# Optimization experiments

Hardware: AMD Instinct MI355X
Metric: run time of the kernel (lower is better)

Reference implementation:

```python
import jax, jax.numpy as jnp
import numpy as np

D_MODEL, D_STATE, D_EVENT, BATCH = 2048, 16, 32, 2048


def setup_inputs() -> dict:
    key = jax.random.key(0)
    ks = jax.random.split(key, 16)
    s = lambda k, sh, scale=0.02: jax.random.normal(k, sh, dtype=jnp.float32) * scale
    # A_log init as in torch: log(idx/d_state*0.5 + 0.05), expanded over d_model
    idx = jnp.arange(1, D_STATE + 1, dtype=jnp.float32)
    A_log = jnp.broadcast_to(jnp.log(idx / D_STATE * 0.5 + 0.05)[None, :], (D_MODEL, D_STATE)).copy()
    return {
        "x_t": jax.random.normal(ks[0], (BATCH, D_MODEL), dtype=jnp.float32),
        "h_prev": jax.random.normal(ks[1], (BATCH, D_MODEL, D_STATE), dtype=jnp.float32),
        "event_t": jax.random.normal(ks[2], (BATCH, D_EVENT), dtype=jnp.float32),
        "A_log": A_log,
        "D": jnp.ones((D_MODEL,), dtype=jnp.float32),
        "Wd": s(ks[3], (D_MODEL, D_MODEL)),
        "bd": jax.random.uniform(ks[4], (D_MODEL,), minval=-2.0, maxval=-1.0, dtype=jnp.float32),
        "We": s(ks[5], (D_MODEL, D_EVENT)),
        "B_W1": s(ks[6], (2 * D_STATE, D_MODEL)),
        "B_b1": jnp.zeros((2 * D_STATE,), dtype=jnp.float32),
        "B_W2": s(ks[7], (D_STATE, 2 * D_STATE)),
        "B_b2": jnp.zeros((D_STATE,), dtype=jnp.float32),
        "B_We": s(ks[8], (D_STATE, D_EVENT)),
        "A_We": s(ks[9], (D_MODEL, D_EVENT)),
        "C_W": s(ks[10], (D_STATE, D_MODEL)),
    }


def reference(x_t, h_prev, event_t, A_log, D, Wd, bd, We, B_W1, B_b1, B_W2, B_b2, B_We, A_We, C_W):
    # event-modulated step size: (B, d_model)
    delta = jax.nn.softplus(x_t @ Wd.T + bd + event_t @ We.T)
    # input-to-state matrix: (B, d_state)
    B_t = jax.nn.silu(x_t @ B_W1.T + B_b1) @ B_W2.T + B_b2 + event_t @ B_We.T
    C_t = x_t @ C_W.T  # (B, d_state)
    A_base = -jnp.exp(jnp.clip(A_log, -3.0, 1.0))[None]        # (1, d_model, d_state)
    event_pole = (event_t @ A_We.T)[..., None]                  # (B, d_model, 1)
    A_eff = A_base + event_pole                                 # (B, d_model, d_state)
    delta_safe = jnp.minimum(delta, 2.0)[..., None]             # (B, d_model, 1)
    A_bar = jnp.exp(delta_safe * A_eff)
    B_bar = delta_safe * B_t[:, None, :]                        # (B, d_model, d_state)
    h_t = A_bar * h_prev + B_bar * x_t[..., None]
    y_t = jnp.einsum('bdn,bn->bd', h_t, C_t) + D * x_t
    return (y_t, h_t)
```

## Files before the change

### kernel.cpp

```cpp
#include <hip/hip_runtime.h>
#include <math.h>

#define D_MODEL 2048
#define D_STATE 16
#define D_EVENT 32
#define BATCH   2048

typedef __attribute__((ext_vector_type(4))) float f32x4;
typedef __attribute__((ext_vector_type(8))) short short8;
typedef __attribute__((ext_vector_type(8))) __bf16 bf16x8;
typedef __attribute__((ext_vector_type(4))) unsigned short us4;

__device__ inline unsigned short f2bf(float f) {
  unsigned int u = __builtin_bit_cast(unsigned int, f);
  u += 0x7fffu + ((u >> 16) & 1u);
  return (unsigned short)(u >> 16);
}

__global__ __launch_bounds__(256) void prep_kernel(
    const float* __restrict__ x, const float* __restrict__ wd,
    const float* __restrict__ ev, const float* __restrict__ we,
    const float* __restrict__ alog,
    unsigned short* __restrict__ xb, unsigned short* __restrict__ wdb,
    unsigned short* __restrict__ evb, unsigned short* __restrict__ web,
    float* __restrict__ abase)
{
  const int t = blockIdx.x * 256 + threadIdx.x;
  if (t < (BATCH * D_MODEL) / 4) {
    f32x4 v = *(const f32x4*)(x + (size_t)t * 4);
    f32x4 w = *(const f32x4*)(wd + (size_t)t * 4);
    us4 ov, ow;
#pragma unroll
    for (int r = 0; r < 4; ++r) { ov[r] = f2bf(v[r]); ow[r] = f2bf(w[r]); }
    *(us4*)(xb + (size_t)t * 4) = ov;
    *(us4*)(wdb + (size_t)t * 4) = ow;
  }
  if (t < (BATCH * D_EVENT) / 4) {
    f32x4 e = *(const f32x4*)(ev + (size_t)t * 4);
    f32x4 s = *(const f32x4*)(we + (size_t)t * 4);
    us4 oe, os;
#pragma unroll
    for (int r = 0; r < 4; ++r) { oe[r] = f2bf(e[r]); os[r] = f2bf(s[r]); }
    *(us4*)(evb + (size_t)t * 4) = oe;
    *(us4*)(web + (size_t)t * 4) = os;
  }
  if (t < (D_MODEL * D_STATE) / 4) {
    f32x4 a = *(const f32x4*)(alog + (size_t)t * 4);
    f32x4 o;
#pragma unroll
    for (int r = 0; r < 4; ++r) {
      float c = fminf(fmaxf(a[r], -3.0f), 1.0f);
      o[r] = -expf(c);
    }
    *(f32x4*)(abase + (size_t)t * 4) = o;
  }
}

__global__ __launch_bounds__(256) void bc_kernel(
    const float* __restrict__ x, const float* __restrict__ ev,
    const float* __restrict__ BW1, const float* __restrict__ Bb1,
    const float* __restrict__ BW2, const float* __restrict__ Bb2,
    const float* __restrict__ BWe, const float* __restrict__ CW,
    float* __restrict__ Bt, float* __restrict__ Ct)
{
  __shared__ float xs[D_MODEL];
  __shared__ float t1s[2 * D_STATE];
  const int b = blockIdx.x, tid = threadIdx.x;
  f32x4* xs4 = (f32x4*)xs;
  const f32x4* xg = (const f32x4*)(x + (size_t)b * D_MODEL);
  xs4[tid] = xg[tid];
  xs4[tid + 256] = xg[tid + 256];
  __syncthreads();
  const int wave = tid >> 6, lane = tid & 63;
#pragma unroll 1
  for (int jj = 0; jj < 12; ++jj) {
    const int j = wave * 12 + jj;
    const float* wr = (j < 32) ? (BW1 + (size_t)j * D_MODEL)
                               : (CW + (size_t)(j - 32) * D_MODEL);
    float s = 0.f;
    for (int k = lane; k < D_MODEL; k += 64) s += xs[k] * wr[k];
#pragma unroll
    for (int o = 32; o > 0; o >>= 1) s += __shfl_xor(s, o);
    if (lane == 0) {
      if (j < 32) {
        float z = s + Bb1[j];
        t1s[j] = z / (1.f + expf(-z));
      } else {
        Ct[b * D_STATE + (j - 32)] = s;
      }
    }
  }
  __syncthreads();
  if (tid < D_STATE) {
    const int n = tid;
    float s = Bb2[n];
    const float* w2 = BW2 + n * (2 * D_STATE);
    const float* we = BWe + n * D_EVENT;
    const float* eb = ev + (size_t)b * D_EVENT;
#pragma unroll
    for (int k = 0; k < 2 * D_STATE; ++k) s += t1s[k] * w2[k];
#pragma unroll
    for (int k = 0; k < D_EVENT; ++k) s += eb[k] * we[k];
    Bt[b * D_STATE + n] = s;
  }
}

__device__ inline void gld_lds16(const unsigned short* g, unsigned short* l) {
  __builtin_amdgcn_global_load_lds(
      (const __attribute__((address_space(1))) unsigned int*)g,
      (__attribute__((address_space(3))) unsigned int*)l, 16, 0, 0);
}

__global__ __launch_bounds__(256) void gemm_delta(
    const unsigned short* __restrict__ xb, const unsigned short* __restrict__ wdb,
    const unsigned short* __restrict__ evb, const unsigned short* __restrict__ web,
    const float* __restrict__ bd, float* __restrict__ delta)
{
  __shared__ unsigned short As[128 * 32];
  __shared__ unsigned short Bs[128 * 32];
  const int tid = threadIdx.x;
  const int wave = tid >> 6, lane = tid & 63;
  const int r16 = lane & 15, q = lane >> 4;
  const int b0 = blockIdx.y * 128, d0 = blockIdx.x * 128;
  const int wm = (wave >> 1) * 64, wn = (wave & 1) * 64;
  const int srow = tid >> 2, skp = tid & 3;
  f32x4 acc[4][4] = {};

  for (int kt = 0; kt < D_MODEL / 32; ++kt) {
    const int k0 = kt * 32;
#pragma unroll
    for (int c = 0; c < 2; ++c) {
      gld_lds16(xb + (size_t)(b0 + srow + c * 64) * D_MODEL + k0 + skp * 8,
                As + c * 2048 + wave * 512);
      gld_lds16(wdb + (size_t)(d0 + srow + c * 64) * D_MODEL + k0 + skp * 8,
                Bs + c * 2048 + wave * 512);
    }
    __syncthreads();
    bf16x8 af[4], bf[4];
#pragma unroll
    for (int i = 0; i < 4; ++i) {
      af[i] = __builtin_bit_cast(bf16x8, *(const short8*)(As + (wm + i * 16 + r16) * 32 + q * 8));
      bf[i] = __builtin_bit_cast(bf16x8, *(const short8*)(Bs + (wn + i * 16 + r16) * 32 + q * 8));
    }
#pragma unroll
    for (int i = 0; i < 4; ++i)
#pragma unroll
      for (int j = 0; j < 4; ++j)
        acc[i][j] = __builtin_amdgcn_mfma_f32_16x16x32_bf16(af[i], bf[j], acc[i][j], 0, 0, 0);
    __syncthreads();
  }
  {
#pragma unroll
    for (int c = 0; c < 2; ++c) {
      gld_lds16(evb + (size_t)(b0 + srow + c * 64) * D_EVENT + skp * 8,
                As + c * 2048 + wave * 512);
      gld_lds16(web + (size_t)(d0 + srow + c * 64) * D_EVENT + skp * 8,
                Bs + c * 2048 + wave * 512);
    }
    __syncthreads();
    bf16x8 af[4], bf[4];
#pragma unroll
    for (int i = 0; i < 4; ++i) {
      af[i] = __builtin_bit_cast(bf16x8, *(const short8*)(As + (wm + i * 16 + r16) * 32 + q * 8));
      bf[i] = __builtin_bit_cast(bf16x8, *(const short8*)(Bs + (wn + i * 16 + r16) * 32 + q * 8));
    }
#pragma unroll
    for (int i = 0; i < 4; ++i)
#pragma unroll
      for (int j = 0; j < 4; ++j)
        acc[i][j] = __builtin_amdgcn_mfma_f32_16x16x32_bf16(af[i], bf[j], acc[i][j], 0, 0, 0);
  }
#pragma unroll
  for (int j = 0; j < 4; ++j) {
    const int d = d0 + wn + j * 16 + r16;
    const float bdv = bd[d];
#pragma unroll
    for (int i = 0; i < 4; ++i) {
      const int brow = b0 + wm + i * 16 + q * 4;
#pragma unroll
      for (int r = 0; r < 4; ++r) {
        float pre = acc[i][j][r] + bdv;
        float sp = fmaxf(pre, 0.f) + log1pf(__expf(-fabsf(pre)));
        delta[(size_t)(brow + r) * D_MODEL + d] = fminf(sp, 2.0f);
      }
    }
  }
}

__global__ __launch_bounds__(256) void update_kernel(
    const float* __restrict__ hprev, const float* __restrict__ x,
    const float* __restrict__ ev, const float* __restrict__ AWe,
    const float* __restrict__ Dv,
    const float* __restrict__ delta, const float* __restrict__ abase,
    const float* __restrict__ Bt, const float* __restrict__ Ct,
    float* __restrict__ y, float* __restrict__ h)
{
  const int t = blockIdx.x * 256 + threadIdx.x;
  const int pid = t >> 2, qq = t & 3;
  const int b = pid >> 11, d = pid & (D_MODEL - 1);

  f32x4 hp = *(const f32x4*)(hprev + (size_t)pid * D_STATE + qq * 4);
  f32x4 ab = *(const f32x4*)(abase + d * D_STATE + qq * 4);
  f32x4 bt = *(const f32x4*)(Bt + b * D_STATE + qq * 4);
  f32x4 ct = *(const f32x4*)(Ct + b * D_STATE + qq * 4);
  const float dlt = delta[pid];
  const float xv = x[pid];

  const float* evp = ev + (size_t)b * D_EVENT + qq * 8;
  const float* awp = AWe + (size_t)d * D_EVENT + qq * 8;
  f32x4 e0 = *(const f32x4*)evp, e1 = *(const f32x4*)(evp + 4);
  f32x4 a0 = *(const f32x4*)awp, a1 = *(const f32x4*)(awp + 4);
  float p = e0[0]*a0[0] + e0[1]*a0[1] + e0[2]*a0[2] + e0[3]*a0[3]
          + e1[0]*a1[0] + e1[1]*a1[1] + e1[2]*a1[2] + e1[3]*a1[3];
  p += __shfl_xor(p, 1);
  p += __shfl_xor(p, 2);

  const float dl2 = dlt * 1.4426950408889634f;
  const float bx = dlt * xv;
  f32x4 hn;
  float yp = 0.f;
#pragma unroll
  for (int r = 0; r < 4; ++r) {
    float abar = exp2f(dl2 * (ab[r] + p));
    float hv = abar * hp[r] + bx * bt[r];
    hn[r] = hv;
    yp += hv * ct[r];
  }
  *(f32x4*)(h + (size_t)pid * D_STATE + qq * 4) = hn;
  yp += __shfl_xor(yp, 1);
  yp += __shfl_xor(yp, 2);
  if (qq == 0) y[pid] = yp + Dv[d] * xv;
}

extern "C" void kernel_launch(void* const* d_in, const int* in_sizes, int n_in,
                              void* d_out, int out_size, void* d_ws, size_t ws_size,
                              hipStream_t stream) {
  const float* x     = (const float*)d_in[0];
  const float* hprev = (const float*)d_in[1];
  const float* ev    = (const float*)d_in[2];
  const float* alog  = (const float*)d_in[3];
  const float* Dv    = (const float*)d_in[4];
  const float* Wd    = (const float*)d_in[5];
  const float* bd    = (const float*)d_in[6];
  const float* We    = (const float*)d_in[7];
  const float* BW1   = (const float*)d_in[8];
  const float* Bb1   = (const float*)d_in[9];
  const float* BW2   = (const float*)d_in[10];
  const float* Bb2   = (const float*)d_in[11];
  const float* BWe   = (const float*)d_in[12];
  const float* AWe   = (const float*)d_in[13];
  const float* CW    = (const float*)d_in[14];

  float* y = (float*)d_out;
  float* h = (float*)d_out + (size_t)BATCH * D_MODEL;

  char* ws = (char*)d_ws;
  unsigned short* xb  = (unsigned short*)(ws);
  unsigned short* wdb = (unsigned short*)(ws + (8u << 20));
  float* delta        = (float*)(ws + (16u << 20));
  float* Bt           = (float*)(ws + (32u << 20));
  float* Ct           = (float*)(ws + (32u << 20) + (128u << 10));
  float* abase        = (float*)(ws + (32u << 20) + (256u << 10));
  unsigned short* evb = (unsigned short*)(ws + (32u << 20) + (384u << 10));
  unsigned short* web = (unsigned short*)(ws + (32u << 20) + (512u << 10));

  hipLaunchKernelGGL(prep_kernel, dim3((BATCH * D_MODEL) / 4 / 256), dim3(256), 0, stream,
                     x, Wd, ev, We, alog, xb, wdb, evb, web, abase);
  hipLaunchKernelGGL(bc_kernel, dim3(BATCH), dim3(256), 0, stream,
                     x, ev, BW1, Bb1, BW2, Bb2, BWe, CW, Bt, Ct);
  hipLaunchKernelGGL(gemm_delta, dim3(D_MODEL / 128, BATCH / 128), dim3(256), 0, stream,
                     xb, wdb, evb, web, bd, delta);
  hipLaunchKernelGGL(update_kernel, dim3((size_t)BATCH * D_MODEL * 4 / 256), dim3(256), 0, stream,
                     hprev, x, ev, AWe, Dv, delta, abase, Bt, Ct, y, h);
}
```

Baseline: 706.3 us.

## Fuse delta GEMM with state update and compute event pole via MFMA

Merges the delta GEMM and the elementwise state-update kernel into one, so the state update runs in the GEMM epilogue and the delta intermediate no longer round-trips through global memory. The event pole (event_t @ A_We.T) is computed with a second set of bf16 MFMA accumulators instead of per-element FP32 dot products. The M tile is halved to 64 rows with launch_bounds(256,2) to make room for the extra accumulators. The cost is that the epilogue's h_prev loads and h stores are per-lane strided 64-byte rows, which coalesce worse than the old update kernel's, and the pole now carries bf16 rounding error.

```diff
diff --git a/kernel.cpp b/kernel.cpp
--- a/kernel.cpp
+++ b/kernel.cpp
@@ -20,10 +20,10 @@
 __global__ __launch_bounds__(256) void prep_kernel(
     const float* __restrict__ x, const float* __restrict__ wd,
     const float* __restrict__ ev, const float* __restrict__ we,
-    const float* __restrict__ alog,
+    const float* __restrict__ awe, const float* __restrict__ alog,
     unsigned short* __restrict__ xb, unsigned short* __restrict__ wdb,
     unsigned short* __restrict__ evb, unsigned short* __restrict__ web,
-    float* __restrict__ abase)
+    unsigned short* __restrict__ aweb, float* __restrict__ abase)
 {
   const int t = blockIdx.x * 256 + threadIdx.x;
   if (t < (BATCH * D_MODEL) / 4) {
@@ -38,11 +38,13 @@
   if (t < (BATCH * D_EVENT) / 4) {
     f32x4 e = *(const f32x4*)(ev + (size_t)t * 4);
     f32x4 s = *(const f32x4*)(we + (size_t)t * 4);
-    us4 oe, os;
-#pragma unroll
-    for (int r = 0; r < 4; ++r) { oe[r] = f2bf(e[r]); os[r] = f2bf(s[r]); }
+    f32x4 a = *(const f32x4*)(awe + (size_t)t * 4);
+    us4 oe, os, oa;
+#pragma unroll
+    for (int r = 0; r < 4; ++r) { oe[r] = f2bf(e[r]); os[r] = f2bf(s[r]); oa[r] = f2bf(a[r]); }
     *(us4*)(evb + (size_t)t * 4) = oe;
     *(us4*)(web + (size_t)t * 4) = os;
+    *(us4*)(aweb + (size_t)t * 4) = oa;
   }
   if (t < (D_MODEL * D_STATE) / 4) {
     f32x4 a = *(const f32x4*)(alog + (size_t)t * 4);
@@ -111,125 +113,113 @@
       (__attribute__((address_space(3))) unsigned int*)l, 16, 0, 0);
 }
 
-__global__ __launch_bounds__(256) void gemm_delta(
+__global__ __launch_bounds__(256, 2) void gemm_update(
     const unsigned short* __restrict__ xb, const unsigned short* __restrict__ wdb,
     const unsigned short* __restrict__ evb, const unsigned short* __restrict__ web,
-    const float* __restrict__ bd, float* __restrict__ delta)
+    const unsigned short* __restrict__ aweb,
+    const float* __restrict__ bd, const float* __restrict__ x,
+    const float* __restrict__ hprev, const float* __restrict__ abase,
+    const float* __restrict__ Bt, const float* __restrict__ Ct,
+    const float* __restrict__ Dv,
+    float* __restrict__ y, float* __restrict__ h)
 {
-  __shared__ unsigned short As[128 * 32];
+  __shared__ unsigned short As[6144];
   __shared__ unsigned short Bs[128 * 32];
   const int tid = threadIdx.x;
   const int wave = tid >> 6, lane = tid & 63;
   const int r16 = lane & 15, q = lane >> 4;
-  const int b0 = blockIdx.y * 128, d0 = blockIdx.x * 128;
-  const int wm = (wave >> 1) * 64, wn = (wave & 1) * 64;
+  const int d0 = blockIdx.x * 128, b0 = blockIdx.y * 64;
+  const int wm = (wave >> 1) * 32, wn = (wave & 1) * 64;
   const int srow = tid >> 2, skp = tid & 3;
-  f32x4 acc[4][4] = {};
+  f32x4 acc[2][4] = {};
+  f32x4 acc2[2][4] = {};
 
   for (int kt = 0; kt < D_MODEL / 32; ++kt) {
     const int k0 = kt * 32;
-#pragma unroll
-    for (int c = 0; c < 2; ++c) {
-      gld_lds16(xb + (size_t)(b0 + srow + c * 64) * D_MODEL + k0 + skp * 8,
-                As + c * 2048 + wave * 512);
-      gld_lds16(wdb + (size_t)(d0 + srow + c * 64) * D_MODEL + k0 + skp * 8,
-                Bs + c * 2048 + wave * 512);
-    }
+    gld_lds16(xb + (size_t)(b0 + srow) * D_MODEL + k0 + skp * 8, As + wave * 512);
+    gld_lds16(wdb + (size_t)(d0 + srow) * D_MODEL + k0 + skp * 8, Bs + wave * 512);
+    gld_lds16(wdb + (size_t)(d0 + 64 + srow) * D_MODEL + k0 + skp * 8, Bs + 2048 + wave * 512);
     __syncthreads();
-    bf16x8 af[4], bf[4];
-#pragma unroll
-    for (int i = 0; i < 4; ++i) {
+    bf16x8 af[2], bf[4];
+#pragma unroll
+    for (int i = 0; i < 2; ++i)
       af[i] = __builtin_bit_cast(bf16x8, *(const short8*)(As + (wm + i * 16 + r16) * 32 + q * 8));
-      bf[i] = __builtin_bit_cast(bf16x8, *(const short8*)(Bs + (wn + i * 16 + r16) * 32 + q * 8));
-    }
-#pragma unroll
-    for (int i = 0; i < 4; ++i)
+#pragma unroll
+    for (int j = 0; j < 4; ++j)
+      bf[j] = __builtin_bit_cast(bf16x8, *(const short8*)(Bs + (wn + j * 16 + r16) * 32 + q * 8));
+#pragma unroll
+    for (int i = 0; i < 2; ++i)
 #pragma unroll
       for (int j = 0; j < 4; ++j)
         acc[i][j] = __builtin_amdgcn_mfma_f32_16x16x32_bf16(af[i], bf[j], acc[i][j], 0, 0, 0);
     __syncthreads();
   }
   {
-#pragma unroll
-    for (int c = 0; c < 2; ++c) {
-      gld_lds16(evb + (size_t)(b0 + srow + c * 64) * D_EVENT + skp * 8,
-                As + c * 2048 + wave * 512);
-      gld_lds16(web + (size_t)(d0 + srow + c * 64) * D_EVENT + skp * 8,
-                Bs + c * 2048 + wave * 512);
-    }
+    gld_lds16(evb + (size_t)(b0 + srow) * D_EVENT + skp * 8, As + wave * 512);
+    gld_lds16(web + (size_t)(d0 + srow) * D_EVENT + skp * 8, Bs + wave * 512);
+    gld_lds16(web + (size_t)(d0 + 64 + srow) * D_EVENT + skp * 8, Bs + 2048 + wave * 512);
+    gld_lds16(aweb + (size_t)(d0 + srow) * D_EVENT + skp * 8, As + 2048 + wave * 512);
+    gld_lds16(aweb + (size_t)(d0 + 64 + srow) * D_EVENT + skp * 8, As + 4096 + wave * 512);
     __syncthreads();
-    bf16x8 af[4], bf[4];
-#pragma unroll
-    for (int i = 0; i < 4; ++i) {
+    bf16x8 af[2], bf[4], bfa[4];
+#pragma unroll
+    for (int i = 0; i < 2; ++i)
       af[i] = __builtin_bit_cast(bf16x8, *(const short8*)(As + (wm + i * 16 + r16) * 32 + q * 8));
-      bf[i] = __builtin_bit_cast(bf16x8, *(const short8*)(Bs + (wn + i * 16 + r16) * 32 + q * 8));
-    }
-#pragma unroll
-    for (int i = 0; i < 4; ++i)
-#pragma unroll
-      for (int j = 0; j < 4; ++j)
-        acc[i][j] = __builtin_amdgcn_mfma_f32_16x16x32_bf16(af[i], bf[j], acc[i][j], 0, 0, 0);
+#pragma unroll
+    for (int j = 0; j < 4; ++j) {
+      bf[j]  = __builtin_bit_cast(bf16x8, *(const short8*)(Bs + (wn + j * 16 + r16) * 32 + q * 8));
+      bfa[j] = __builtin_bit_cast(bf16x8, *(const short8*)(As + 2048 + (wn + j * 16 + r16) * 32 + q * 8));
+    }
+#pragma unroll
+    for (int i = 0; i < 2; ++i)
+#pragma unroll
+      for (int j = 0; j < 4; ++j) {
+        acc[i][j]  = __builtin_amdgcn_mfma_f32_16x16x32_bf16(af[i], bf[j],  acc[i][j],  0, 0, 0);
+        acc2[i][j] = __builtin_amdgcn_mfma_f32_16x16x32_bf16(af[i], bfa[j], acc2[i][j], 0, 0, 0);
+      }
   }
 #pragma unroll
   for (int j = 0; j < 4; ++j) {
     const int d = d0 + wn + j * 16 + r16;
     const float bdv = bd[d];
-#pragma unroll
-    for (int i = 0; i < 4; ++i) {
-      const int brow = b0 + wm + i * 16 + q * 4;
+    const float Dd = Dv[d];
+    const f32x4* ab4 = (const f32x4*)(abase + (size_t)d * D_STATE);
+    f32x4 ab0 = ab4[0], ab1 = ab4[1], ab2 = ab4[2], ab3 = ab4[3];
+#pragma unroll
+    for (int i = 0; i < 2; ++i) {
 #pragma unroll
       for (int r = 0; r < 4; ++r) {
+        const int b = b0 + wm + i * 16 + q * 4 + r;
+        const size_t pid = (size_t)b * D_MODEL + d;
         float pre = acc[i][j][r] + bdv;
         float sp = fmaxf(pre, 0.f) + log1pf(__expf(-fabsf(pre)));
-        delta[(size_t)(brow + r) * D_MODEL + d] = fminf(sp, 2.0f);
+        float dlt = fminf(sp, 2.0f);
+        const float pole = acc2[i][j][r];
+        const float xv = x[pid];
+        const float dl2 = dlt * 1.4426950408889634f;
+        const float bx = dlt * xv;
+        const f32x4* hp4 = (const f32x4*)(hprev + pid * D_STATE);
+        const f32x4* bt4 = (const f32x4*)(Bt + (size_t)b * D_STATE);
+        const f32x4* ct4 = (const f32x4*)(Ct + (size_t)b * D_STATE);
+        f32x4* hn4 = (f32x4*)(h + pid * D_STATE);
+        const f32x4 abv[4] = {ab0, ab1, ab2, ab3};
+        float yp = 0.f;
+#pragma unroll
+        for (int s = 0; s < 4; ++s) {
+          f32x4 hp = hp4[s], bt = bt4[s], ct = ct4[s], ab = abv[s], hn;
+#pragma unroll
+          for (int u = 0; u < 4; ++u) {
+            float abar = exp2f(dl2 * (ab[u] + pole));
+            float hv = abar * hp[u] + bx * bt[u];
+            hn[u] = hv;
+            yp += hv * ct[u];
+          }
+          hn4[s] = hn;
+        }
+        y[pid] = yp + Dd * xv;
       }
     }
   }
-}
-
-__global__ __launch_bounds__(256) void update_kernel(
-    const float* __restrict__ hprev, const float* __restrict__ x,
-    const float* __restrict__ ev, const float* __restrict__ AWe,
-    const float* __restrict__ Dv,
-    const float* __restrict__ delta, const float* __restrict__ abase,
-    const float* __restrict__ Bt, const float* __restrict__ Ct,
-    float* __restrict__ y, float* __restrict__ h)
-{
-  const int t = blockIdx.x * 256 + threadIdx.x;
-  const int pid = t >> 2, qq = t & 3;
-  const int b = pid >> 11, d = pid & (D_MODEL - 1);
-
-  f32x4 hp = *(const f32x4*)(hprev + (size_t)pid * D_STATE + qq * 4);
-  f32x4 ab = *(const f32x4*)(abase + d * D_STATE + qq * 4);
-  f32x4 bt = *(const f32x4*)(Bt + b * D_STATE + qq * 4);
-  f32x4 ct = *(const f32x4*)(Ct + b * D_STATE + qq * 4);
-  const float dlt = delta[pid];
-  const float xv = x[pid];
-
-  const float* evp = ev + (size_t)b * D_EVENT + qq * 8;
-  const float* awp = AWe + (size_t)d * D_EVENT + qq * 8;
-  f32x4 e0 = *(const f32x4*)evp, e1 = *(const f32x4*)(evp + 4);
-  f32x4 a0 = *(const f32x4*)awp, a1 = *(const f32x4*)(awp + 4);
-  float p = e0[0]*a0[0] + e0[1]*a0[1] + e0[2]*a0[2] + e0[3]*a0[3]
-          + e1[0]*a1[0] + e1[1]*a1[1] + e1[2]*a1[2] + e1[3]*a1[3];
-  p += __shfl_xor(p, 1);
-  p += __shfl_xor(p, 2);
-
-  const float dl2 = dlt * 1.4426950408889634f;
-  const float bx = dlt * xv;
-  f32x4 hn;
-  float yp = 0.f;
-#pragma unroll
-  for (int r = 0; r < 4; ++r) {
-    float abar = exp2f(dl2 * (ab[r] + p));
-    float hv = abar * hp[r] + bx * bt[r];
-    hn[r] = hv;
-    yp += hv * ct[r];
-  }
-  *(f32x4*)(h + (size_t)pid * D_STATE + qq * 4) = hn;
-  yp += __shfl_xor(yp, 1);
-  yp += __shfl_xor(yp, 2);
-  if (qq == 0) y[pid] = yp + Dv[d] * xv;
 }
 
 extern "C" void kernel_launch(void* const* d_in, const int* in_sizes, int n_in,
@@ -255,21 +245,19 @@
   float* h = (float*)d_out + (size_t)BATCH * D_MODEL;
 
   char* ws = (char*)d_ws;
-  unsigned short* xb  = (unsigned short*)(ws);
-  unsigned short* wdb = (unsigned short*)(ws + (8u << 20));
-  float* delta        = (float*)(ws + (16u << 20));
-  float* Bt           = (float*)(ws + (32u << 20));
-  float* Ct           = (float*)(ws + (32u << 20) + (128u << 10));
-  float* abase        = (float*)(ws + (32u << 20) + (256u << 10));
-  unsigned short* evb = (unsigned short*)(ws + (32u << 20) + (384u << 10));
-  unsigned short* web = (unsigned short*)(ws + (32u << 20) + (512u << 10));
+  unsigned short* xb   = (unsigned short*)(ws);
+  unsigned short* wdb  = (unsigned short*)(ws + (8u << 20));
+  float* Bt            = (float*)(ws + (16u << 20));
+  float* Ct            = (float*)(ws + (16u << 20) + (128u << 10));
+  float* abase         = (float*)(ws + (16u << 20) + (256u << 10));
+  unsigned short* evb  = (unsigned short*)(ws + (16u << 20) + (384u << 10));
+  unsigned short* web  = (unsigned short*)(ws + (16u << 20) + (512u << 10));
+  unsigned short* aweb = (unsigned short*)(ws + (16u << 20) + (640u << 10));
 
   hipLaunchKernelGGL(prep_kernel, dim3((BATCH * D_MODEL) / 4 / 256), dim3(256), 0, stream,
-                     x, Wd, ev, We, alog, xb, wdb, evb, web, abase);
+                     x, Wd, ev, We, AWe, alog, xb, wdb, evb, web, aweb, abase);
   hipLaunchKernelGGL(bc_kernel, dim3(BATCH), dim3(256), 0, stream,
                      x, ev, BW1, Bb1, BW2, Bb2, BWe, CW, Bt, Ct);
-  hipLaunchKernelGGL(gemm_delta, dim3(D_MODEL / 128, BATCH / 128), dim3(256), 0, stream,
-                     xb, wdb, evb, web, bd, delta);
-  hipLaunchKernelGGL(update_kernel, dim3((size_t)BATCH * D_MODEL * 4 / 256), dim3(256), 0, stream,
-                     hprev, x, ev, AWe, Dv, delta, abase, Bt, Ct, y, h);
-}
+  hipLaunchKernelGGL(gemm_update, dim3(D_MODEL / 128, BATCH / 64), dim3(256), 0, stream,
+                     xb, wdb, evb, web, aweb, bd, x, hprev, abase, Bt, Ct, Dv, y, h);
+}
```

Measured after the change: 942.7 us. +33.5%, slower.
